# Kernel optimization log

Hardware: AMD Instinct MI355X
Metric: run time of the kernel (lower is better)

Reference implementation:

```python
import jax, jax.numpy as jnp
import numpy as np

N = 50000          # nodes
E = 1_600_000      # edges (avg degree 32)
F_IN = 128         # num_node_features
HID = 128          # hidden_dim
G = 512            # graphs in batch
NEG_SLOPE = 0.2    # PyG GATConv default


def setup_inputs() -> dict:
    key = jax.random.key(0)
    ks = jax.random.split(key, 13)
    s_in = 1.0 / np.sqrt(F_IN)
    s_h = 1.0 / np.sqrt(HID)
    return {
        "x": jax.random.normal(ks[0], (N, F_IN), jnp.float32),
        "edge_index": jax.random.randint(ks[1], (2, E), 0, N, dtype=jnp.int32),
        "batch": jnp.sort(jax.random.randint(ks[2], (N,), 0, G, dtype=jnp.int32)),
        "W1": jax.random.normal(ks[3], (F_IN, HID), jnp.float32) * s_in,
        "a_src1": jax.random.normal(ks[4], (HID,), jnp.float32) * s_h,
        "a_dst1": jax.random.normal(ks[5], (HID,), jnp.float32) * s_h,
        "b1": jnp.zeros((HID,), jnp.float32),
        "W2": jax.random.normal(ks[6], (HID, HID), jnp.float32) * s_h,
        "a_src2": jax.random.normal(ks[7], (HID,), jnp.float32) * s_h,
        "a_dst2": jax.random.normal(ks[8], (HID,), jnp.float32) * s_h,
        "b2": jnp.zeros((HID,), jnp.float32),
        "fc_w": jax.random.normal(ks[9], (2 * HID, 1), jnp.float32) * (1.0 / np.sqrt(2 * HID)),
        "fc_b": jnp.zeros((1,), jnp.float32),
    }


def _gat_conv(x, W, a_src, a_dst, b, src, dst, n):
    # PyG GATConv, heads=1: h = xW; alpha_e = softmax_dst(leaky_relu(a_s.h[src] + a_d.h[dst]))
    h = x @ W                                    # [N, C]
    asrc = h @ a_src                             # [N]
    adst = h @ a_dst                             # [N]
    logits = jax.nn.leaky_relu(asrc[src] + adst[dst], NEG_SLOPE)  # [E']
    m = jax.ops.segment_max(logits, dst, num_segments=n)
    ex = jnp.exp(logits - m[dst])
    denom = jax.ops.segment_sum(ex, dst, num_segments=n)
    alpha = ex / denom[dst]                      # segment softmax over incoming edges
    out = jax.ops.segment_sum(h[src] * alpha[:, None], dst, num_segments=n)
    return out + b


def reference(x, edge_index, batch, W1, a_src1, a_dst1, b1, W2, a_src2, a_dst2, b2, fc_w, fc_b):
    n = x.shape[0]
    loop = jnp.arange(n, dtype=edge_index.dtype)   # add_self_loops=True (PyG default)
    src = jnp.concatenate([edge_index[0], loop])
    dst = jnp.concatenate([edge_index[1], loop])

    h = jax.nn.relu(x)
    h = jax.nn.relu(_gat_conv(h, W1, a_src1, a_dst1, b1, src, dst, n))
    h = jax.nn.relu(_gat_conv(h, W2, a_src2, a_dst2, b2, src, dst, n))

    counts = jax.ops.segment_sum(jnp.ones((n,), h.dtype), batch, num_segments=G)
    maxp = jax.ops.segment_max(h, batch, num_segments=G)
    maxp = jnp.where(counts[:, None] > 0, maxp, 0.0)
    meanp = jax.ops.segment_sum(h, batch, num_segments=G) / jnp.maximum(counts, 1.0)[:, None]
    pooled = jnp.concatenate([maxp, meanp], axis=1)  # [G, 2*HID]
    return pooled @ fc_w + fc_b                      # [G, 1]
```

## Files before the change

kernel.cpp:

```cpp
#include <hip/hip_runtime.h>
#include <math.h>


#define LEAKY 0.2f
#define CAP 128
#define CSTRIDE 16

typedef short bf16x8 __attribute__((ext_vector_type(8)));
typedef float f32x4 __attribute__((ext_vector_type(4)));

__device__ __forceinline__ unsigned short f2bf(float x) {
    unsigned int u = __float_as_uint(x);
    unsigned int r = (u + 0x7FFFu + ((u >> 16) & 1u)) >> 16;
    return (unsigned short)r;
}
__device__ __forceinline__ float bf2f(unsigned short b) {
    return __uint_as_float((unsigned int)b << 16);
}

__global__ __launch_bounds__(256, 5) void gemmscat(
        const float* __restrict__ A,
        const float* __restrict__ W,
        unsigned short* __restrict__ Cb,
        const float* __restrict__ a_src,
        const float* __restrict__ a_dst,
        float* __restrict__ asv,
        float* __restrict__ adv,
        int n, int applyRelu, int gemmBlocks,
        const int* __restrict__ ei,
        int* __restrict__ cnt,
        unsigned short* __restrict__ col,
        int E) {
    __shared__ __align__(16) unsigned short Bt[2][64 * 128];

    if ((int)blockIdx.x >= gemmBlocks) {
        const int b = (int)blockIdx.x - gemmBlocks;
        const int g = (int)blockIdx.x & 7;
        const int lo = (int)(((long long)n * g) >> 3);
        const int hi = (int)(((long long)n * (g + 1)) >> 3);
        const int base = (b >> 3) * 4096;
        int4 dv[4], sv[4];
        int ok[4];
#pragma unroll
        for (int t = 0; t < 4; ++t) {
            int i0 = base + t * 1024 + (int)threadIdx.x * 4;
            ok[t] = (i0 < E);
            if (ok[t]) {
                dv[t] = *(const int4*)(ei + (size_t)E + i0);
                sv[t] = *(const int4*)(ei + i0);
            }
        }
#pragma unroll
        for (int t = 0; t < 4; ++t) {
            if (!ok[t]) continue;
            int dd[4] = { dv[t].x, dv[t].y, dv[t].z, dv[t].w };
            int ss[4] = { sv[t].x, sv[t].y, sv[t].z, sv[t].w };
#pragma unroll
            for (int j = 0; j < 4; ++j) {
                int d = dd[j];
                if (d >= lo && d < hi) {
                    int pos = atomicAdd(&cnt[(size_t)d * CSTRIDE], 1);
                    if (pos < CAP) col[(size_t)d * CAP + pos] = (unsigned short)ss[j];
                }
            }
        }
        return;
    }

    const int tid = threadIdx.x;
    const int wv = tid >> 6;
    const int lane = tid & 63;
    const int cl = lane & 15;
    const int kg = lane >> 4;

    const int row0 = blockIdx.x * 64;
    const int row = row0 + wv * 16 + cl;
    bf16x8 ahi[4], alo[4];
#pragma unroll
    for (int ks = 0; ks < 4; ++ks) {
        int k0 = ks * 32 + kg * 8;
        float vv[8] = {0.f, 0.f, 0.f, 0.f, 0.f, 0.f, 0.f, 0.f};
        if (row < n) {
            float4 v0 = *(const float4*)(A + (size_t)row * 128 + k0);
            float4 v1 = *(const float4*)(A + (size_t)row * 128 + k0 + 4);
            vv[0] = v0.x; vv[1] = v0.y; vv[2] = v0.z; vv[3] = v0.w;
            vv[4] = v1.x; vv[5] = v1.y; vv[6] = v1.z; vv[7] = v1.w;
            if (applyRelu) {
#pragma unroll
                for (int u = 0; u < 8; ++u) vv[u] = fmaxf(vv[u], 0.f);
            }
        }
#pragma unroll
        for (int u = 0; u < 8; ++u) {
            unsigned short h = f2bf(vv[u]);
            ahi[ks][u] = (short)h;
            alo[ks][u] = (short)f2bf(vv[u] - bf2f(h));
        }
    }

    f32x4 acc[8];
#pragma unroll
    for (int ci = 0; ci < 8; ++ci) {
        acc[ci][0] = 0.f; acc[ci][1] = 0.f; acc[ci][2] = 0.f; acc[ci][3] = 0.f;
    }

#pragma unroll
    for (int h = 0; h < 2; ++h) {
        __syncthreads();
        {
            int c64 = tid & 63;
            int c = h * 64 + c64;
            int kh = tid >> 6;
#pragma unroll
            for (int j = 0; j < 4; ++j) {
                int kb = kh * 32 + j * 8;
                unsigned short thi[8], tlo[8];
#pragma unroll
                for (int u = 0; u < 8; ++u) {
                    float v = W[(size_t)(kb + u) * 128 + c];
                    unsigned short hh = f2bf(v);
                    thi[u] = hh;
                    tlo[u] = f2bf(v - bf2f(hh));
                }
                int byteoff = (c64 * 256 + kb * 2) ^ ((c64 & 7) << 4);
                *(uint4*)((char*)Bt[0] + byteoff) = *(const uint4*)thi;
                *(uint4*)((char*)Bt[1] + byteoff) = *(const uint4*)tlo;
            }
        }
        __syncthreads();
#pragma unroll
        for (int ks = 0; ks < 4; ++ks) {
            int k0 = ks * 32 + kg * 8;
#pragma unroll
            for (int ct = 0; ct < 4; ++ct) {
                int c64 = ct * 16 + cl;
                int byteoff = (c64 * 256 + k0 * 2) ^ ((c64 & 7) << 4);
                bf16x8 bhi = *(const bf16x8*)((const char*)Bt[0] + byteoff);
                bf16x8 blo = *(const bf16x8*)((const char*)Bt[1] + byteoff);
                int ci = h * 4 + ct;
                acc[ci] = __builtin_amdgcn_mfma_f32_16x16x32_bf16(
                    ahi[ks], bhi, acc[ci], 0, 0, 0);
                acc[ci] = __builtin_amdgcn_mfma_f32_16x16x32_bf16(
                    ahi[ks], blo, acc[ci], 0, 0, 0);
                acc[ci] = __builtin_amdgcn_mfma_f32_16x16x32_bf16(
                    alo[ks], bhi, acc[ci], 0, 0, 0);
            }
        }
    }

    {
        float ps[4] = {0.f, 0.f, 0.f, 0.f};
        float pd[4] = {0.f, 0.f, 0.f, 0.f};
#pragma unroll
        for (int ci = 0; ci < 8; ++ci) {
            float as_ = a_src[ci * 16 + cl];
            float ad_ = a_dst[ci * 16 + cl];
#pragma unroll
            for (int r = 0; r < 4; ++r) {
                ps[r] += acc[ci][r] * as_;
                pd[r] += acc[ci][r] * ad_;
            }
        }
#pragma unroll
        for (int r = 0; r < 4; ++r) {
#pragma unroll
            for (int off = 1; off < 16; off <<= 1) {
                ps[r] += __shfl_xor(ps[r], off, 64);
                pd[r] += __shfl_xor(pd[r], off, 64);
            }
        }
        if (cl == 0) {
#pragma unroll
            for (int r = 0; r < 4; ++r) {
                int rr = row0 + wv * 16 + kg * 4 + r;
                if (rr < n) { asv[rr] = ps[r]; adv[rr] = pd[r]; }
            }
        }
    }

    __syncthreads();
    unsigned short* Cst = Bt[0];
#pragma unroll
    for (int ci = 0; ci < 8; ++ci) {
#pragma unroll
        for (int r = 0; r < 4; ++r)
            Cst[(wv * 16 + kg * 4 + r) * 128 + ci * 16 + cl] = f2bf(acc[ci][r]);
    }
    __syncthreads();
    {
        int r = tid >> 2, cb = (tid & 3) * 32;
        int grow = row0 + r;
        if (grow < n) {
            uint4* dst = (uint4*)(Cb + (size_t)grow * 128 + cb);
            const uint4* src = (const uint4*)(Cst + r * 128 + cb);
            dst[0] = src[0]; dst[1] = src[1]; dst[2] = src[2]; dst[3] = src[3];
        }
    }
}

__global__ __launch_bounds__(256) void aggregate(const unsigned short* __restrict__ hb,
                                                 const int* __restrict__ cnt,
                                                 const unsigned short* __restrict__ col,
                                                 const float* __restrict__ asv,
                                                 const float* __restrict__ adv,
                                                 const float* __restrict__ bias,
                                                 float* __restrict__ out, int n) {
    __shared__ int   scol[4][128];
    __shared__ float swt[4][128];
    const int wv = threadIdx.x >> 6;
    const int lane = threadIdx.x & 63;
    const int w = blockIdx.x * 4 + wv;
    if (w >= n) return;
    int deg = cnt[(size_t)w * CSTRIDE];
    if (deg > CAP - 1) deg = CAP - 1;
    const int D = deg + 1;
    const size_t start = (size_t)w * CAP;
    const float ad = adv[w];

    int c0 = 0, c1 = 0;
    float l0 = -INFINITY, l1 = -INFINITY;
    if (lane < D) {
        c0 = (lane < deg) ? (int)col[start + lane] : w;
        l0 = asv[c0] + ad;
        l0 = l0 > 0.f ? l0 : LEAKY * l0;
    }
    if (64 + lane < D) {
        c1 = (64 + lane < deg) ? (int)col[start + 64 + lane] : w;
        l1 = asv[c1] + ad;
        l1 = l1 > 0.f ? l1 : LEAKY * l1;
    }
    float m = fmaxf(l0, l1);
#pragma unroll
    for (int off = 32; off; off >>= 1) m = fmaxf(m, __shfl_xor(m, off, 64));
    float e0 = (lane < D) ? __expf(l0 - m) : 0.f;
    float e1 = (64 + lane < D) ? __expf(l1 - m) : 0.f;
    float s = e0 + e1;
#pragma unroll
    for (int off = 32; off; off >>= 1) s += __shfl_xor(s, off, 64);
    float inv = 1.f / s;
    if (lane < D)      { scol[wv][lane] = c0;      swt[wv][lane] = e0; }
    if (64 + lane < D) { scol[wv][64 + lane] = c1; swt[wv][64 + lane] = e1; }

    const int hw = lane >> 5;
    const int sl = lane & 31;
    float4 aa[8];
#pragma unroll
    for (int j = 0; j < 8; ++j) aa[j] = make_float4(0.f, 0.f, 0.f, 0.f);
    for (int i = 0; i < D; i += 16) {
        int cs[8]; float ws[8];
#pragma unroll
        for (int j = 0; j < 8; ++j) {
            int idx = i + 2 * j + hw;
            int cl = idx < D ? idx : D - 1;
            cs[j] = scol[wv][cl];
            ws[j] = (idx < D) ? swt[wv][idx] : 0.f;
        }
        ushort4 rs[8];
#pragma unroll
        for (int j = 0; j < 8; ++j)
            rs[j] = *((const ushort4*)(hb + (size_t)cs[j] * 128) + sl);
#pragma unroll
        for (int j = 0; j < 8; ++j) {
            aa[j].x += ws[j] * bf2f(rs[j].x);
            aa[j].y += ws[j] * bf2f(rs[j].y);
            aa[j].z += ws[j] * bf2f(rs[j].z);
            aa[j].w += ws[j] * bf2f(rs[j].w);
        }
    }
#pragma unroll
    for (int j = 1; j < 8; ++j) {
        aa[0].x += aa[j].x; aa[0].y += aa[j].y;
        aa[0].z += aa[j].z; aa[0].w += aa[j].w;
    }
    aa[0].x += __shfl_xor(aa[0].x, 32);
    aa[0].y += __shfl_xor(aa[0].y, 32);
    aa[0].z += __shfl_xor(aa[0].z, 32);
    aa[0].w += __shfl_xor(aa[0].w, 32);
    if (hw == 0) {
        float4 b = ((const float4*)bias)[sl];
        float4 o;
        o.x = fmaxf(aa[0].x * inv + b.x, 0.f);
        o.y = fmaxf(aa[0].y * inv + b.y, 0.f);
        o.z = fmaxf(aa[0].z * inv + b.z, 0.f);
        o.w = fmaxf(aa[0].w * inv + b.w, 0.f);
        *((float4*)(out + (size_t)w * 128) + sl) = o;
    }
}

__global__ __launch_bounds__(128) void poolfc(const float* __restrict__ h2,
                                              const int* __restrict__ batch,
                                              const float* __restrict__ fcw,
                                              const float* __restrict__ fcb,
                                              float* __restrict__ out, int G, int n) {
    __shared__ int seg[2];
    int g = blockIdx.x;
    int f = threadIdx.x;
    if (f < 2) {
        int target = g + f;
        int lo = 0, hi = n;
        while (lo < hi) {
            int mid = (lo + hi) >> 1;
            if (batch[mid] < target) lo = mid + 1; else hi = mid;
        }
        seg[f] = lo;
    }
    __syncthreads();
    int s = seg[0], e = seg[1];
    float m = -INFINITY, sum = 0.f;
    for (int node = s; node < e; ++node) {
        float v = h2[(size_t)node * 128 + f];
        m = fmaxf(m, v);
        sum += v;
    }
    int cnt = e - s;
    float maxp = (cnt > 0) ? m : 0.f;
    float cden = (float)(cnt > 0 ? cnt : 1);
    float meanp = sum / cden;
    float p = maxp * fcw[f] + meanp * fcw[128 + f];
    __shared__ float red[128];
    red[f] = p;
    __syncthreads();
    for (int off = 64; off; off >>= 1) {
        if (f < off) red[f] += red[f + off];
        __syncthreads();
    }
    if (f == 0) out[g] = red[0] + fcb[0];
}

extern "C" void kernel_launch(void* const* d_in, const int* in_sizes, int n_in,
                              void* d_out, int out_size, void* d_ws, size_t ws_size,
                              hipStream_t stream) {
    const int N = in_sizes[0] / 128;
    const int E = in_sizes[1] / 2;
    const int G = out_size;

    const float* x      = (const float*)d_in[0];
    const int*   ei     = (const int*)d_in[1];
    const int*   batch  = (const int*)d_in[2];
    const float* W1     = (const float*)d_in[3];
    const float* a_src1 = (const float*)d_in[4];
    const float* a_dst1 = (const float*)d_in[5];
    const float* b1     = (const float*)d_in[6];
    const float* W2     = (const float*)d_in[7];
    const float* a_src2 = (const float*)d_in[8];
    const float* a_dst2 = (const float*)d_in[9];
    const float* b2     = (const float*)d_in[10];
    const float* fcw    = (const float*)d_in[11];
    const float* fcb    = (const float*)d_in[12];
    float* out = (float*)d_out;

    char* wp = (char*)d_ws;
    auto alloc = [&](size_t bytes) -> void* {
        void* p = (void*)wp;
        wp += (bytes + 255) & ~(size_t)255;
        return p;
    };
    int* cnt     = (int*)alloc(sizeof(int) * (size_t)N * CSTRIDE);
    unsigned short* col = (unsigned short*)alloc(sizeof(unsigned short) * (size_t)N * CAP);
    float* ha    = (float*)alloc(sizeof(float) * (size_t)N * 128);
    unsigned short* hb = (unsigned short*)alloc(sizeof(unsigned short) * (size_t)N * 128);
    float* asv   = (float*)alloc(sizeof(float) * N);
    float* adv   = (float*)alloc(sizeof(float) * N);

    hipMemsetAsync(cnt, 0, sizeof(int) * (size_t)N * CSTRIDE, stream);

    const int gemmGrid = (N + 63) / 64;
    const int waveGrid = (N + 3) / 4;
    const int scatGrid = ((E + 4095) / 4096) * 8;

    gemmscat<<<gemmGrid + scatGrid, 256, 0, stream>>>(
        x, W1, hb, a_src1, a_dst1, asv, adv, N, 1, gemmGrid, ei, cnt, col, E);
    aggregate<<<waveGrid, 256, 0, stream>>>(hb, cnt, col, asv, adv, b1, ha, N);

    gemmscat<<<gemmGrid, 256, 0, stream>>>(
        ha, W2, hb, a_src2, a_dst2, asv, adv, N, 0, gemmGrid, ei, cnt, col, E);
    aggregate<<<waveGrid, 256, 0, stream>>>(hb, cnt, col, asv, adv, b2, ha, N);

    poolfc<<<G, 128, 0, stream>>>(ha, batch, fcw, fcb, out, G, N);
}
```

Measured before the change: 352.0 us.

## Replace global atomic CSR scatter with two-pass bucketed binning

Edge-to-CSR construction no longer does one global atomic per edge on padded per-node counters across 8 partitioned passes. Each block now bins its edges into 512-node buckets using shared-memory atomics, reserves space with one global atomic per bucket, and writes packed (dst,src) words. A new binbuild kernel then scatters each bucket into per-node column lists with shared atomics. This cuts global atomic traffic and the memset of the large padded count array, at the cost of an extra kernel launch, an intermediate buffer pass, and a fixed bucket capacity that could drop edges on skewed graphs.

```diff
diff --git a/kernel.cpp b/kernel.cpp
--- a/kernel.cpp
+++ b/kernel.cpp
@@ -4,7 +4,7 @@
 
 #define LEAKY 0.2f
 #define CAP 128
-#define CSTRIDE 16
+#define CAPB 20480
 
 typedef short bf16x8 __attribute__((ext_vector_type(8)));
 typedef float f32x4 __attribute__((ext_vector_type(4)));
@@ -28,40 +28,59 @@
         float* __restrict__ adv,
         int n, int applyRelu, int gemmBlocks,
         const int* __restrict__ ei,
-        int* __restrict__ cnt,
-        unsigned short* __restrict__ col,
+        int* __restrict__ binCnt,
+        unsigned* __restrict__ binBuf,
         int E) {
     __shared__ __align__(16) unsigned short Bt[2][64 * 128];
 
     if ((int)blockIdx.x >= gemmBlocks) {
-        const int b = (int)blockIdx.x - gemmBlocks;
-        const int g = (int)blockIdx.x & 7;
-        const int lo = (int)(((long long)n * g) >> 3);
-        const int hi = (int)(((long long)n * (g + 1)) >> 3);
-        const int base = (b >> 3) * 4096;
+        int* lcnt  = (int*)Bt;
+        int* gbase = ((int*)Bt) + 128;
+        const int bb = (int)blockIdx.x - gemmBlocks;
+        const int base = bb * 4096;
+        const int tid = threadIdx.x;
+        const int nbins = (n + 511) >> 9;
+        if (tid < nbins) lcnt[tid] = 0;
+        __syncthreads();
+
         int4 dv[4], sv[4];
         int ok[4];
 #pragma unroll
         for (int t = 0; t < 4; ++t) {
-            int i0 = base + t * 1024 + (int)threadIdx.x * 4;
+            int i0 = base + t * 1024 + tid * 4;
             ok[t] = (i0 < E);
             if (ok[t]) {
                 dv[t] = *(const int4*)(ei + (size_t)E + i0);
                 sv[t] = *(const int4*)(ei + i0);
             }
         }
+        int rr[16];
+        unsigned pk[16];
 #pragma unroll
         for (int t = 0; t < 4; ++t) {
-            if (!ok[t]) continue;
             int dd[4] = { dv[t].x, dv[t].y, dv[t].z, dv[t].w };
             int ss[4] = { sv[t].x, sv[t].y, sv[t].z, sv[t].w };
 #pragma unroll
-            for (int j = 0; j < 4; ++j) {
-                int d = dd[j];
-                if (d >= lo && d < hi) {
-                    int pos = atomicAdd(&cnt[(size_t)d * CSTRIDE], 1);
-                    if (pos < CAP) col[(size_t)d * CAP + pos] = (unsigned short)ss[j];
+            for (int q = 0; q < 4; ++q) {
+                int j = t * 4 + q;
+                rr[j] = -1;
+                if (ok[t]) {
+                    unsigned d = (unsigned)dd[q];
+                    pk[j] = (d << 16) | (unsigned)ss[q];
+                    rr[j] = atomicAdd(&lcnt[d >> 9], 1);
                 }
+            }
+        }
+        __syncthreads();
+        if (tid < nbins)
+            gbase[tid] = (lcnt[tid] > 0) ? atomicAdd(&binCnt[tid], lcnt[tid]) : 0;
+        __syncthreads();
+#pragma unroll
+        for (int j = 0; j < 16; ++j) {
+            if (rr[j] >= 0) {
+                int b = (int)(pk[j] >> 25);
+                int pos = gbase[b] + rr[j];
+                if (pos < CAPB) binBuf[(size_t)b * CAPB + pos] = pk[j];
             }
         }
         return;
@@ -196,6 +215,30 @@
             dst[0] = src[0]; dst[1] = src[1]; dst[2] = src[2]; dst[3] = src[3];
         }
     }
+}
+
+__global__ __launch_bounds__(512) void binbuild(const unsigned* __restrict__ binBuf,
+                                                const int* __restrict__ binCnt,
+                                                unsigned short* __restrict__ col,
+                                                int* __restrict__ cnt, int n) {
+    __shared__ int lc[512];
+    const int b = blockIdx.x;
+    const int lo = b << 9;
+    const int tid = threadIdx.x;
+    lc[tid] = 0;
+    __syncthreads();
+    int m = binCnt[b];
+    if (m > CAPB) m = CAPB;
+    for (int i = tid; i < m; i += 512) {
+        unsigned u = binBuf[(size_t)b * CAPB + i];
+        int d = (int)(u >> 16);
+        int s = (int)(u & 0xFFFFu);
+        int p = atomicAdd(&lc[d - lo], 1);
+        if (p < CAP) col[(size_t)d * CAP + p] = (unsigned short)s;
+    }
+    __syncthreads();
+    int d = lo + tid;
+    if (d < n) cnt[d] = lc[tid];
 }
 
 __global__ __launch_bounds__(256) void aggregate(const unsigned short* __restrict__ hb,
@@ -211,7 +254,7 @@
     const int lane = threadIdx.x & 63;
     const int w = blockIdx.x * 4 + wv;
     if (w >= n) return;
-    int deg = cnt[(size_t)w * CSTRIDE];
+    int deg = cnt[w];
     if (deg > CAP - 1) deg = CAP - 1;
     const int D = deg + 1;
     const size_t start = (size_t)w * CAP;
@@ -349,31 +392,38 @@
     const float* fcb    = (const float*)d_in[12];
     float* out = (float*)d_out;
 
+    const int NBINS = (N + 511) >> 9;
+
     char* wp = (char*)d_ws;
     auto alloc = [&](size_t bytes) -> void* {
         void* p = (void*)wp;
         wp += (bytes + 255) & ~(size_t)255;
         return p;
     };
-    int* cnt     = (int*)alloc(sizeof(int) * (size_t)N * CSTRIDE);
+    int* cnt        = (int*)alloc(sizeof(int) * N);
+    int* binCnt     = (int*)alloc(sizeof(int) * 128);
+    unsigned* binBuf = (unsigned*)alloc(sizeof(unsigned) * (size_t)NBINS * CAPB);
     unsigned short* col = (unsigned short*)alloc(sizeof(unsigned short) * (size_t)N * CAP);
     float* ha    = (float*)alloc(sizeof(float) * (size_t)N * 128);
     unsigned short* hb = (unsigned short*)alloc(sizeof(unsigned short) * (size_t)N * 128);
     float* asv   = (float*)alloc(sizeof(float) * N);
     float* adv   = (float*)alloc(sizeof(float) * N);
 
-    hipMemsetAsync(cnt, 0, sizeof(int) * (size_t)N * CSTRIDE, stream);
+    hipMemsetAsync(binCnt, 0, sizeof(int) * 128, stream);
 
     const int gemmGrid = (N + 63) / 64;
     const int waveGrid = (N + 3) / 4;
-    const int scatGrid = ((E + 4095) / 4096) * 8;
-
-    gemmscat<<<gemmGrid + scatGrid, 256, 0, stream>>>(
-        x, W1, hb, a_src1, a_dst1, asv, adv, N, 1, gemmGrid, ei, cnt, col, E);
+    const int binGrid  = (E + 4095) / 4096;
+
+    gemmscat<<<gemmGrid + binGrid, 256, 0, stream>>>(
+        x, W1, hb, a_src1, a_dst1, asv, adv, N, 1, gemmGrid, ei,
+        binCnt, binBuf, E);
+    binbuild<<<NBINS, 512, 0, stream>>>(binBuf, binCnt, col, cnt, N);
     aggregate<<<waveGrid, 256, 0, stream>>>(hb, cnt, col, asv, adv, b1, ha, N);
 
     gemmscat<<<gemmGrid, 256, 0, stream>>>(
-        ha, W2, hb, a_src2, a_dst2, asv, adv, N, 0, gemmGrid, ei, cnt, col, E);
+        ha, W2, hb, a_src2, a_dst2, asv, adv, N, 0, gemmGrid, ei,
+        binCnt, binBuf, E);
     aggregate<<<waveGrid, 256, 0, stream>>>(hb, cnt, col, asv, adv, b2, ha, N);
 
     poolfc<<<G, 128, 0, stream>>>(ha, batch, fcw, fcb, out, G, N);
```

Measured after the change: 319.8 us (median of 2 runs). 1.1x faster.
